# Kernel optimization log

Measured on AMD Instinct MI355X. Metric: run time of the kernel, lower is better.

Reference implementation:

```python
import jax, jax.numpy as jnp
import numpy as np
import math

EPS_NORM = 1e-6
EPS_COS = 1e-6
B, L, LC = 2, 2048, 1024
D_MODEL, D_CROSS, D_HEAD = 1024, 1024, 64
N_HEADS = D_MODEL // D_HEAD


def setup_inputs() -> dict:
    key = jax.random.key(0)
    ks = jax.random.split(key, 6)
    x = jax.random.normal(ks[0], (B, L, D_MODEL), jnp.float32)
    pos = jax.random.uniform(ks[1], (B, L, 2), dtype=jnp.float32)  # normalized 2D canvas coords
    x_cross = jax.random.normal(ks[2], (B, LC, D_CROSS), jnp.float32)
    norm_scale = jnp.ones((D_MODEL,), jnp.float32)          # RMSNorm scale (init ones)
    norm_cross_scale = jnp.ones((D_CROSS,), jnp.float32)
    q_w = jax.random.normal(ks[3], (D_MODEL, D_MODEL), jnp.float32) / math.sqrt(D_MODEL)
    kv_w = jax.random.normal(ks[4], (D_CROSS, 2 * D_MODEL), jnp.float32) / math.sqrt(D_CROSS)
    # out_proj is zero-init in the original; use small random weights so the block is non-trivial
    out_w = jax.random.normal(ks[5], (D_MODEL, D_MODEL), jnp.float32) / math.sqrt(D_MODEL)
    scale = jnp.full((N_HEADS,), 10.0, jnp.float32)          # learned per-head cosine-sim scale
    # AxialRoPE2D freqs (k-diffusion style, learnable_freqs=False): [n_heads, d_head//4]
    log_min, log_max = math.log(math.pi), math.log(10.0 * math.pi)
    freqs = jnp.exp(jnp.linspace(log_min, log_max, N_HEADS * D_HEAD // 4 + 1)[:-1])
    freqs = freqs.reshape(D_HEAD // 4, N_HEADS).T            # [H, E//4]
    return dict(x=x, pos=pos, x_cross=x_cross, norm_scale=norm_scale,
                norm_cross_scale=norm_cross_scale, q_w=q_w, kv_w=kv_w,
                scale=scale, out_w=out_w, freqs=freqs)


def _rms_norm(x, scale, eps=EPS_NORM):
    ms = jnp.mean(jnp.square(x), axis=-1, keepdims=True)
    return x * (scale * jax.lax.rsqrt(ms + eps))


def reference(x, pos, x_cross, norm_scale, norm_cross_scale, q_w, kv_w, scale, out_w, freqs):
    skip = x
    xn = _rms_norm(x, norm_scale)
    xc = _rms_norm(x_cross, norm_cross_scale)
    q = xn @ q_w                                             # [B,L,D]
    kv = xc @ kv_w                                           # [B,LC,2D]
    q = q.reshape(B, L, N_HEADS, D_HEAD).transpose(0, 2, 1, 3)      # [B,H,L,E]
    kv = kv.reshape(B, LC, 2, N_HEADS, D_HEAD)               # split (t nh e), t outermost
    k = kv[:, :, 0].transpose(0, 2, 1, 3)                    # [B,H,LC,E]
    v = kv[:, :, 1].transpose(0, 2, 1, 3)
    # per-head cosine-sim QK scaling
    sq = jnp.sqrt(scale)[:, None, None]                      # [H,1,1]
    q = q * (sq * jax.lax.rsqrt(jnp.sum(jnp.square(q), -1, keepdims=True) + EPS_COS))
    k = k * (sq * jax.lax.rsqrt(jnp.sum(jnp.square(k), -1, keepdims=True) + EPS_COS))
    # axial 2D RoPE on q only (as in the original forward)
    theta = jnp.concatenate([pos[..., None, 0:1] * freqs,
                             pos[..., None, 1:2] * freqs], -1)      # [B,L,H,E//2]
    theta = jnp.moveaxis(theta, -2, -3)                      # [B,H,L,E//2]
    d = theta.shape[-1]
    q1, q2 = q[..., :d], q[..., d:]
    cos, sin = jnp.cos(theta), jnp.sin(theta)
    q = jnp.concatenate([q1 * cos - q2 * sin, q2 * cos + q1 * sin], -1)
    # SDPA with scale=1.0 (cosine-sim scaling already applied)
    attn = jax.nn.softmax(jnp.einsum('bhqe,bhke->bhqk', q, k), axis=-1)
    o = jnp.einsum('bhqk,bhke->bhqe', attn, v)
    o = o.transpose(0, 2, 1, 3).reshape(B, L, D_MODEL)       # merge heads
    return o @ out_w + skip
```

## Files before the change

kernel.cpp:

```cpp
#include <hip/hip_runtime.h>
#include <math.h>

typedef unsigned short u16;
typedef __bf16 bf16x8 __attribute__((ext_vector_type(8)));
typedef float f32x4 __attribute__((ext_vector_type(4)));

#define EPS_NORM 1e-6f
#define EPS_COS  1e-6f

static constexpr int Bc = 2;
static constexpr int Lq = 2048;
static constexpr int Lc = 1024;
static constexpr int Dm = 1024;
static constexpr int DH = 64;
static constexpr int NH = 16;

#define F32MODE(probe) ((probe)[0] == 0x3F800000u)

__device__ __forceinline__ float b2f(u16 u) {
  union { unsigned u; float f; } x; x.u = ((unsigned)u) << 16; return x.f;
}
__device__ __forceinline__ u16 f2b(float f) {
  union { float f; unsigned u; } x; x.f = f;
  unsigned v = x.u;
  v += 0x7fffu + ((v >> 16) & 1u);
  return (u16)(v >> 16);
}
__device__ __forceinline__ unsigned pkbf(float lo, float hi) {
#if __has_builtin(__builtin_amdgcn_cvt_pk_bf16_f32)
  return __builtin_bit_cast(unsigned, __builtin_amdgcn_cvt_pk_bf16_f32(lo, hi));
#else
  return (unsigned)f2b(lo) | ((unsigned)f2b(hi) << 16);
#endif
}
__device__ __forceinline__ float loadf(const void* p, size_t i, bool f32m) {
  return f32m ? ((const float*)p)[i] : b2f(((const u16*)p)[i]);
}
__device__ __forceinline__ void gll16(const u16* g, u16* l) {
  __builtin_amdgcn_global_load_lds(
      (const __attribute__((address_space(1))) unsigned*)g,
      (__attribute__((address_space(3))) unsigned*)l, 16, 0, 0);
}

__global__ __launch_bounds__(256) void prep_kernel(
    const void* __restrict__ qw, const void* __restrict__ kvw,
    const void* __restrict__ outw, u16* __restrict__ wqw,
    u16* __restrict__ wkvw, u16* __restrict__ woutw,
    const void* __restrict__ x, const void* __restrict__ xcr,
    const void* __restrict__ nsc, const void* __restrict__ ncs,
    u16* __restrict__ xn, u16* __restrict__ xc,
    const unsigned* __restrict__ probe) {
  bool f32m = F32MODE(probe);
  int id = blockIdx.x;
  int t = threadIdx.x;
  if (id < 6144) {
    int row = id;
    const void* src; const void* sc; u16* dst;
    if (row < Bc * Lq) { src = x; sc = nsc; dst = xn; }
    else { row -= Bc * Lq; src = xcr; sc = ncs; dst = xc; }
    float f[4]; float ss = 0.f;
    if (f32m) {
      float4 a = *(const float4*)((const float*)src + (size_t)row * Dm + t * 4);
      f[0] = a.x; f[1] = a.y; f[2] = a.z; f[3] = a.w;
    } else {
      union { uint2 u2; u16 s[4]; } v;
      v.u2 = *(const uint2*)((const u16*)src + (size_t)row * Dm + t * 4);
#pragma unroll
      for (int i = 0; i < 4; i++) f[i] = b2f(v.s[i]);
    }
#pragma unroll
    for (int i = 0; i < 4; i++) ss += f[i] * f[i];
#pragma unroll
    for (int o = 32; o > 0; o >>= 1) ss += __shfl_xor(ss, o, 64);
    __shared__ float red[4];
    if ((t & 63) == 0) red[t >> 6] = ss;
    __syncthreads();
    float inv = rsqrtf((red[0] + red[1] + red[2] + red[3]) / (float)Dm + EPS_NORM);
    union { uint2 u2; u16 s[4]; } ov;
#pragma unroll
    for (int i = 0; i < 4; i++) ov.s[i] = f2b(f[i] * loadf(sc, t * 4 + i, f32m) * inv);
    *(uint2*)(dst + (size_t)row * Dm + t * 4) = ov.u2;
  } else {
    id -= 6144;
    __shared__ u16 tile[32][33];
    const void* src; u16* dst; int N;
    if (id < 1024)      { src = qw;   dst = wqw;   N = Dm; }
    else if (id < 3072) { src = kvw;  dst = wkvw;  N = 2 * Dm; id -= 1024; }
    else                { src = outw; dst = woutw; N = Dm;     id -= 3072; }
    int k0 = (id & 31) * 32, n0 = (id >> 5) * 32;
    int tn = t & 31, tg = t >> 5;
#pragma unroll
    for (int r = 0; r < 4; r++) {
      int k = tg * 4 + r;
      tile[k][tn] = f2b(loadf(src, (size_t)(k0 + k) * N + n0 + tn, f32m));
    }
    __syncthreads();
#pragma unroll
    for (int r = 0; r < 4; r++) {
      int n = tg * 4 + r;
      dst[(size_t)(n0 + n) * Dm + k0 + tn] = tile[tn][n];
    }
  }
}

__device__ __forceinline__ void gemm_body(
    const u16* __restrict__ A, const u16* __restrict__ Bt,
    int M, int N, int m0, int n0, int mode,
    u16* __restrict__ outb, u16* __restrict__ kfp, u16* __restrict__ vt,
    const void* __restrict__ skip, void* __restrict__ Cn,
    const void* __restrict__ scale, const void* __restrict__ pos,
    const void* __restrict__ freqs, bool f32m,
    u16 (&As)[2][8192], u16 (&Bs)[2][4096]) {
  constexpr int K = Dm;
  int t = threadIdx.x;
  int wv = t >> 6, lane = t & 63;
  int r16 = lane & 15, quad = lane >> 4;

  const u16* pA[4]; const u16* pB[2]; int iLA[4], iLB[2];
#pragma unroll
  for (int c = 0; c < 4; c++) {
    int i = c * 256 + t;
    int row = i >> 3, g = (i & 7) ^ (row & 7);
    pA[c] = A + (size_t)(m0 + row) * K + g * 8;
    iLA[c] = (c * 256 + wv * 64) * 8;
  }
#pragma unroll
  for (int c = 0; c < 2; c++) {
    int i = c * 256 + t;
    int row = i >> 3, g = (i & 7) ^ (row & 7);
    pB[c] = Bt + (size_t)(n0 + row) * K + g * 8;
    iLB[c] = (c * 256 + wv * 64) * 8;
  }

  int offA[2][2], offB[2][4];
#pragma unroll
  for (int kh = 0; kh < 2; kh++) {
    int pa = ((kh * 4 + quad) ^ (r16 & 7)) * 8;
#pragma unroll
    for (int i = 0; i < 2; i++) offA[kh][i] = (wv * 32 + i * 16 + r16) * 64 + pa;
#pragma unroll
    for (int j = 0; j < 4; j++) offB[kh][j] = (j * 16 + r16) * 64 + pa;
  }

  f32x4 acc[2][4] = {};

#pragma unroll
  for (int c = 0; c < 4; c++) gll16(pA[c], &As[0][iLA[c]]);
#pragma unroll
  for (int c = 0; c < 2; c++) gll16(pB[c], &Bs[0][iLB[c]]);

  int niter = K >> 6;
  for (int it = 0; it < niter; ++it) {
    __syncthreads();
    if (it + 1 < niter) {
      int koff = (it + 1) << 6;
      int nb = (it + 1) & 1;
#pragma unroll
      for (int c = 0; c < 4; c++) gll16(pA[c] + koff, &As[nb][iLA[c]]);
#pragma unroll
      for (int c = 0; c < 2; c++) gll16(pB[c] + koff, &Bs[nb][iLB[c]]);
    }
    const u16* Ab = As[it & 1];
    const u16* Bb = Bs[it & 1];
#pragma unroll
    for (int kh = 0; kh < 2; kh++) {
      bf16x8 af[2], bf[4];
#pragma unroll
      for (int i = 0; i < 2; i++)
        af[i] = __builtin_bit_cast(bf16x8, *(const uint4*)(Ab + offA[kh][i]));
#pragma unroll
      for (int j = 0; j < 4; j++)
        bf[j] = __builtin_bit_cast(bf16x8, *(const uint4*)(Bb + offB[kh][j]));
#pragma unroll
      for (int mt = 0; mt < 2; mt++)
#pragma unroll
        for (int nt = 0; nt < 4; nt++)
          acc[mt][nt] = __builtin_amdgcn_mfma_f32_16x16x32_bf16(
              af[mt], bf[nt], acc[mt][nt], 0, 0, 0);
    }
  }

  if (mode == 2) {
#pragma unroll
    for (int mt = 0; mt < 2; mt++)
#pragma unroll
      for (int nt = 0; nt < 4; nt++)
#pragma unroll
        for (int r = 0; r < 4; r++) {
          int m = m0 + wv * 32 + mt * 16 + quad * 4 + r;
          int n = n0 + nt * 16 + r16;
          size_t idx = (size_t)m * N + n;
          float v = acc[mt][nt][r] + loadf(skip, idx, f32m);
          if (f32m) ((float*)Cn)[idx] = v;
          else      outb[idx] = f2b(v);
        }
    return;
  }

  if (mode == 1 && n0 >= Dm) {
    int hh = (n0 - Dm) >> 6;
#pragma unroll
    for (int mt = 0; mt < 2; mt++)
#pragma unroll
      for (int r = 0; r < 4; r++) {
        int m = m0 + wv * 32 + mt * 16 + quad * 4 + r;
        int bb = m >> 10, lc = m & (Lc - 1);
        u16* tb = vt + ((size_t)(bb * NH + hh) * 16 + (lc >> 6)) * 4096;
        int kin = lc & 63;
#pragma unroll
        for (int nt = 0; nt < 4; nt++) {
          int d = nt * 16 + r16;
          tb[d * 64 + ((kin >> 3) ^ (d & 7)) * 8 + (kin & 7)] = f2b(acc[mt][nt][r]);
        }
      }
    return;
  }

  int hh = (n0 & (Dm - 1)) >> 6;
  float sqs = sqrtf(loadf(scale, hh, f32m));
  float fr = (mode == 0) ? loadf(freqs, hh * 16 + r16, f32m) : 0.f;
#pragma unroll
  for (int mt = 0; mt < 2; mt++) {
    float ss[4];
#pragma unroll
    for (int r = 0; r < 4; r++) {
      ss[r] = 0.f;
#pragma unroll
      for (int nt = 0; nt < 4; nt++) ss[r] += acc[mt][nt][r] * acc[mt][nt][r];
    }
#pragma unroll
    for (int o = 1; o < 16; o <<= 1)
#pragma unroll
      for (int r = 0; r < 4; r++) ss[r] += __shfl_xor(ss[r], o, 64);
#pragma unroll
    for (int r = 0; r < 4; r++) {
      int m = m0 + wv * 32 + mt * 16 + quad * 4 + r;
      float inv = sqs * rsqrtf(ss[r] + EPS_COS);
      if (mode == 1) {
        int bb = m >> 10, lc = m & (Lc - 1);
        size_t base = ((size_t)((bb * NH + hh) * Lc) + lc) * 64;
#pragma unroll
        for (int nt = 0; nt < 4; nt++)
          kfp[base + nt * 16 + r16] = f2b(acc[mt][nt][r] * inv);
      } else {
        int bb = m >> 11, l = m & (Lq - 1);
        float p0 = loadf(pos, (size_t)m * 2 + 0, f32m);
        float p1 = loadf(pos, (size_t)m * 2 + 1, f32m);
        size_t base = ((size_t)((bb * NH + hh) * Lq) + l) * 64;
#pragma unroll
        for (int nt = 0; nt < 2; nt++) {
          float th = (nt ? p1 : p0) * fr;
          float c, s;
          sincosf(th, &s, &c);
          float lo = acc[mt][nt][r] * inv, hi = acc[mt][nt + 2][r] * inv;
          outb[base + nt * 16 + r16]       = f2b(lo * c - hi * s);
          outb[base + (nt + 2) * 16 + r16] = f2b(hi * c + lo * s);
        }
      }
    }
  }
}

__global__ __launch_bounds__(256) void qkv_gemm_kernel(
    const u16* __restrict__ xn, const u16* __restrict__ wqw,
    const u16* __restrict__ xc, const u16* __restrict__ wkvw,
    u16* __restrict__ qf, u16* __restrict__ kf, u16* __restrict__ vt,
    const void* __restrict__ scale, const void* __restrict__ pos,
    const void* __restrict__ freqs, const unsigned* __restrict__ probe) {
  __shared__ u16 As[2][8192];
  __shared__ u16 Bs[2][4096];
  bool f32m = F32MODE(probe);
  int blk = blockIdx.x;
  if (blk < 512) {
    gemm_body(xn, wqw, Bc * Lq, Dm, (blk >> 4) * 128, (blk & 15) * 64, 0,
              qf, nullptr, nullptr, nullptr, nullptr, scale, pos, freqs,
              f32m, As, Bs);
  } else {
    int id = blk - 512;
    gemm_body(xc, wkvw, Bc * Lc, 2 * Dm, (id >> 5) * 128, (id & 31) * 64, 1,
              nullptr, kf, vt, nullptr, nullptr, scale, nullptr, nullptr,
              f32m, As, Bs);
  }
}

__global__ __launch_bounds__(256) void final_gemm_kernel(
    const u16* __restrict__ ob, const u16* __restrict__ woutw,
    const void* __restrict__ skip, void* __restrict__ Cn,
    u16* __restrict__ outb, const unsigned* __restrict__ probe) {
  __shared__ u16 As[2][8192];
  __shared__ u16 Bs[2][4096];
  bool f32m = F32MODE(probe);
  int blk = blockIdx.x;
  gemm_body(ob, woutw, Bc * Lq, Dm, (blk >> 4) * 128, (blk & 15) * 64, 2,
            outb, nullptr, nullptr, skip, Cn, nullptr, nullptr, nullptr,
            f32m, As, Bs);
}

__global__ __launch_bounds__(256) void attn_kernel(
    const u16* __restrict__ qf, const u16* __restrict__ kf,
    const u16* __restrict__ vt, u16* __restrict__ o_out,
    const void* __restrict__ scale, const unsigned* __restrict__ probe) {
  __shared__ u16 Kt[2][4096];
  __shared__ u16 Vs[2][4096];
  __shared__ u16 Pl[4][2][1024];

  int blk = blockIdx.x;
  int bh = blk & 31;
  int qt = blk >> 5;
  int h = bh & 15;
  bool f32m = F32MODE(probe);
  float sh = loadf(scale, h, f32m);
  const u16* kbase = kf + (size_t)bh * Lc * DH;
  const u16* vtb   = vt + (size_t)bh * 16 * 4096;
  int t = threadIdx.x;
  int wv = t >> 6, lane = t & 63;
  int r16 = lane & 15, quad = lane >> 4;

  const u16* qb0 = qf + ((size_t)bh * Lq + qt * 128 + wv * 16) * DH;
  const u16* qb1 = qb0 + 64 * DH;
  bf16x8 af00 = __builtin_bit_cast(bf16x8, *(const uint4*)(qb0 + r16 * DH + 0  + quad * 8));
  bf16x8 af01 = __builtin_bit_cast(bf16x8, *(const uint4*)(qb0 + r16 * DH + 32 + quad * 8));
  bf16x8 af10 = __builtin_bit_cast(bf16x8, *(const uint4*)(qb1 + r16 * DH + 0  + quad * 8));
  bf16x8 af11 = __builtin_bit_cast(bf16x8, *(const uint4*)(qb1 + r16 * DH + 32 + quad * 8));

  int e0 = t, e1 = 256 + t;
  int row0 = e0 >> 3, g0 = (e0 & 7) ^ (row0 & 7);
  int row1 = e1 >> 3, g1 = (e1 & 7) ^ (row1 & 7);
  const u16* pK0 = kbase + (size_t)row0 * DH + g0 * 8;
  const u16* pK1 = kbase + (size_t)row1 * DH + g1 * 8;
  const u16* pV0 = vtb + e0 * 8;
  const u16* pV1 = vtb + e1 * 8;
  int iS0 = (wv * 64) * 8, iS1 = (256 + wv * 64) * 8;
  int kphys0 = ((quad)     ^ (r16 & 7)) * 8;
  int kphys1 = ((4 | quad) ^ (r16 & 7)) * 8;

  float l0[4] = {0.f, 0.f, 0.f, 0.f}, l1[4] = {0.f, 0.f, 0.f, 0.f};
  f32x4 oa0[4] = {{0,0,0,0},{0,0,0,0},{0,0,0,0},{0,0,0,0}};
  f32x4 oa1[4] = {{0,0,0,0},{0,0,0,0},{0,0,0,0},{0,0,0,0}};

  gll16(pK0, &Kt[0][iS0]); gll16(pK1, &Kt[0][iS1]);
  gll16(pV0, &Vs[0][iS0]); gll16(pV1, &Vs[0][iS1]);

  for (int it = 0; it < Lc / 64; ++it) {
    __syncthreads();
    if (it + 1 < Lc / 64) {
      size_t koff = (size_t)(it + 1) * 64 * DH;
      size_t voff = (size_t)(it + 1) * 4096;
      int nb = (it + 1) & 1;
      gll16(pK0 + koff, &Kt[nb][iS0]);
      gll16(pK1 + koff, &Kt[nb][iS1]);
      gll16(pV0 + voff, &Vs[nb][iS0]);
      gll16(pV1 + voff, &Vs[nb][iS1]);
    }
    const u16* Kb = Kt[it & 1];
    const u16* Vb = Vs[it & 1];

    f32x4 s0[4], s1[4];
#pragma unroll
    for (int nt = 0; nt < 4; nt++) {
      int nrow = (nt * 16 + r16) * 64;
      bf16x8 bf0 = __builtin_bit_cast(bf16x8, *(const uint4*)(Kb + nrow + kphys0));
      bf16x8 bf1 = __builtin_bit_cast(bf16x8, *(const uint4*)(Kb + nrow + kphys1));
      s0[nt] = (f32x4){0.f, 0.f, 0.f, 0.f};
      s0[nt] = __builtin_amdgcn_mfma_f32_16x16x32_bf16(af00, bf0, s0[nt], 0, 0, 0);
      s0[nt] = __builtin_amdgcn_mfma_f32_16x16x32_bf16(af01, bf1, s0[nt], 0, 0, 0);
      s1[nt] = (f32x4){0.f, 0.f, 0.f, 0.f};
      s1[nt] = __builtin_amdgcn_mfma_f32_16x16x32_bf16(af10, bf0, s1[nt], 0, 0, 0);
      s1[nt] = __builtin_amdgcn_mfma_f32_16x16x32_bf16(af11, bf1, s1[nt], 0, 0, 0);
    }

#pragma unroll
    for (int set = 0; set < 2; set++) {
      u16* P = &Pl[wv][set][0];
#pragma unroll
      for (int r = 0; r < 4; r++) {
        f32x4* s = set ? s1 : s0;
        float p0 = __expf(s[0][r] - sh);
        float p1 = __expf(s[1][r] - sh);
        float p2 = __expf(s[2][r] - sh);
        float p3 = __expf(s[3][r] - sh);
        if (set) l1[r] += (p0 + p1) + (p2 + p3);
        else     l0[r] += (p0 + p1) + (p2 + p3);
        unsigned pa = pkbf(p0, p1), pb = pkbf(p2, p3);
        int mrow = quad * 4 + r;
        int bx = mrow & 7;
        int base = mrow * 64 + (r16 & 7);
        int c0 = (r16 >> 3);
        P[base + ((c0    ) ^ bx) * 8] = (u16)pa;
        P[base + ((c0 + 2) ^ bx) * 8] = (u16)(pa >> 16);
        P[base + ((c0 + 4) ^ bx) * 8] = (u16)pb;
        P[base + ((c0 + 6) ^ bx) * 8] = (u16)(pb >> 16);
      }
    }

#pragma unroll
    for (int dt = 0; dt < 4; dt++) {
      int vrow = (dt * 16 + r16) * 64;
#pragma unroll
      for (int kc = 0; kc < 2; kc++) {
        int ph = kc ? kphys1 : kphys0;
        bf16x8 bu  = __builtin_bit_cast(bf16x8, *(const uint4*)(Vb + vrow + ph));
        bf16x8 au0 = __builtin_bit_cast(bf16x8, *(const uint4*)&Pl[wv][0][r16 * 64 + ph]);
        bf16x8 au1 = __builtin_bit_cast(bf16x8, *(const uint4*)&Pl[wv][1][r16 * 64 + ph]);
        oa0[dt] = __builtin_amdgcn_mfma_f32_16x16x32_bf16(au0, bu, oa0[dt], 0, 0, 0);
        oa1[dt] = __builtin_amdgcn_mfma_f32_16x16x32_bf16(au1, bu, oa1[dt], 0, 0, 0);
      }
    }
  }

  int b = bh >> 4;
#pragma unroll
  for (int set = 0; set < 2; set++) {
    float* lr = set ? l1 : l0;
    f32x4* oa = set ? oa1 : oa0;
    float inv[4];
#pragma unroll
    for (int r = 0; r < 4; r++) {
      float l = lr[r];
#pragma unroll
      for (int o = 8; o > 0; o >>= 1) l += __shfl_xor(l, o, 64);
      inv[r] = 1.f / l;
    }
#pragma unroll
    for (int dt = 0; dt < 4; dt++)
#pragma unroll
      for (int r = 0; r < 4; r++) {
        int m = qt * 128 + set * 64 + wv * 16 + quad * 4 + r;
        o_out[((size_t)(b * Lq + m)) * Dm + h * DH + dt * 16 + r16] =
            f2b(oa[dt][r] * inv[r]);
      }
  }
}

extern "C" void kernel_launch(void* const* d_in, const int* in_sizes, int n_in,
                              void* d_out, int out_size, void* d_ws, size_t ws_size,
                              hipStream_t stream) {
  const void* x     = d_in[0];
  const void* pos   = d_in[1];
  const void* xcr   = d_in[2];
  const void* nsc   = d_in[3];
  const void* ncs   = d_in[4];
  const void* qw    = d_in[5];
  const void* kvw   = d_in[6];
  const void* scale = d_in[7];
  const void* outw  = d_in[8];
  const void* freqs = d_in[9];
  const unsigned* probe = (const unsigned*)nsc;

  char* ws = (char*)d_ws;
  const size_t MB = 1u << 20;
  u16*   wqw  = (u16*)(ws + 0 * MB);
  u16*   wkvw = (u16*)(ws + 2 * MB);
  u16*   woutw= (u16*)(ws + 6 * MB);
  u16*   xn   = (u16*)(ws + 8 * MB);
  u16*   ob   = (u16*)(ws + 8 * MB);
  u16*   xc   = (u16*)(ws + 16 * MB);
  u16*   qf   = (u16*)(ws + 20 * MB);
  u16*   kf   = (u16*)(ws + 28 * MB);
  u16*   vt   = (u16*)(ws + 32 * MB);

  prep_kernel<<<6144 + 4096, 256, 0, stream>>>(
      qw, kvw, outw, wqw, wkvw, woutw, x, xcr, nsc, ncs, xn, xc, probe);
  qkv_gemm_kernel<<<1024, 256, 0, stream>>>(xn, wqw, xc, wkvw, qf, kf, vt,
                                            scale, pos, freqs, probe);
  attn_kernel<<<512, 256, 0, stream>>>(qf, kf, vt, ob, scale, probe);
  final_gemm_kernel<<<512, 256, 0, stream>>>(ob, woutw, x, d_out, (u16*)d_out, probe);
}
```

Measured before the change: 196.0 us.

## Split QKV GEMM into two launches and remap tiles for XCD locality

The fused Q/KV projection kernel becomes two separate launches. The Q, KV and output GEMMs now remap block indices so that blocks dispatched round-robin to the same XCD work on neighbouring M tiles (and, for KV, N tiles). The goal is better L2 reuse of A and B tiles within each XCD's private cache. The price is an extra kernel launch and the loss of Q and KV work running concurrently in one grid.

```diff
diff --git a/kernel.cpp b/kernel.cpp
--- a/kernel.cpp
+++ b/kernel.cpp
@@ -261,26 +261,37 @@
   }
 }
 
-__global__ __launch_bounds__(256) void qkv_gemm_kernel(
+__global__ __launch_bounds__(256) void q_gemm_kernel(
     const u16* __restrict__ xn, const u16* __restrict__ wqw,
-    const u16* __restrict__ xc, const u16* __restrict__ wkvw,
-    u16* __restrict__ qf, u16* __restrict__ kf, u16* __restrict__ vt,
-    const void* __restrict__ scale, const void* __restrict__ pos,
-    const void* __restrict__ freqs, const unsigned* __restrict__ probe) {
+    u16* __restrict__ qf, const void* __restrict__ scale,
+    const void* __restrict__ pos, const void* __restrict__ freqs,
+    const unsigned* __restrict__ probe) {
   __shared__ u16 As[2][8192];
   __shared__ u16 Bs[2][4096];
   bool f32m = F32MODE(probe);
   int blk = blockIdx.x;
-  if (blk < 512) {
-    gemm_body(xn, wqw, Bc * Lq, Dm, (blk >> 4) * 128, (blk & 15) * 64, 0,
-              qf, nullptr, nullptr, nullptr, nullptr, scale, pos, freqs,
-              f32m, As, Bs);
-  } else {
-    int id = blk - 512;
-    gemm_body(xc, wkvw, Bc * Lc, 2 * Dm, (id >> 5) * 128, (id & 31) * 64, 1,
-              nullptr, kf, vt, nullptr, nullptr, scale, nullptr, nullptr,
-              f32m, As, Bs);
-  }
+  int xcd = blk & 7, local = blk >> 3;
+  int mt = xcd * 4 + (local >> 4);
+  int nt = local & 15;
+  gemm_body(xn, wqw, Bc * Lq, Dm, mt * 128, nt * 64, 0,
+            qf, nullptr, nullptr, nullptr, nullptr, scale, pos, freqs,
+            f32m, As, Bs);
+}
+
+__global__ __launch_bounds__(256) void kv_gemm_kernel(
+    const u16* __restrict__ xc, const u16* __restrict__ wkvw,
+    u16* __restrict__ kf, u16* __restrict__ vt,
+    const void* __restrict__ scale, const unsigned* __restrict__ probe) {
+  __shared__ u16 As[2][8192];
+  __shared__ u16 Bs[2][4096];
+  bool f32m = F32MODE(probe);
+  int blk = blockIdx.x;
+  int xcd = blk & 7, local = blk >> 3;
+  int mt = (xcd >> 1) * 4 + (local >> 4);
+  int nt = (xcd & 1) * 16 + (local & 15);
+  gemm_body(xc, wkvw, Bc * Lc, 2 * Dm, mt * 128, nt * 64, 1,
+            nullptr, kf, vt, nullptr, nullptr, scale, nullptr, nullptr,
+            f32m, As, Bs);
 }
 
 __global__ __launch_bounds__(256) void final_gemm_kernel(
@@ -291,7 +302,10 @@
   __shared__ u16 Bs[2][4096];
   bool f32m = F32MODE(probe);
   int blk = blockIdx.x;
-  gemm_body(ob, woutw, Bc * Lq, Dm, (blk >> 4) * 128, (blk & 15) * 64, 2,
+  int xcd = blk & 7, local = blk >> 3;
+  int mt = xcd * 4 + (local >> 4);
+  int nt = local & 15;
+  gemm_body(ob, woutw, Bc * Lq, Dm, mt * 128, nt * 64, 2,
             outb, nullptr, nullptr, skip, Cn, nullptr, nullptr, nullptr,
             f32m, As, Bs);
 }
@@ -461,8 +475,8 @@
 
   prep_kernel<<<6144 + 4096, 256, 0, stream>>>(
       qw, kvw, outw, wqw, wkvw, woutw, x, xcr, nsc, ncs, xn, xc, probe);
-  qkv_gemm_kernel<<<1024, 256, 0, stream>>>(xn, wqw, xc, wkvw, qf, kf, vt,
-                                            scale, pos, freqs, probe);
+  q_gemm_kernel<<<512, 256, 0, stream>>>(xn, wqw, qf, scale, pos, freqs, probe);
+  kv_gemm_kernel<<<512, 256, 0, stream>>>(xc, wkvw, kf, vt, scale, probe);
   attn_kernel<<<512, 256, 0, stream>>>(qf, kf, vt, ob, scale, probe);
   final_gemm_kernel<<<512, 256, 0, stream>>>(ob, woutw, x, d_out, (u16*)d_out, probe);
 }
```

Measured after the change: 204.7 us. 1.04x slower.
